# Kernel tuning notes

Hardware: AMD Instinct MI355X
Metric: run time of the kernel (lower is better)

The kernel has to match this reference:

```python
import jax, jax.numpy as jnp
import numpy as np

B, N, C, DIN, DOUT = 16, 65536, 256, 16, 16  # ratio = N // C = 256 nodes per cluster


def setup_inputs() -> dict:
    key = jax.random.key(0)
    k1, k2, k3, k4, k5 = jax.random.split(key, 5)
    stdv = 1.0 / np.sqrt(DOUT)
    x = jax.random.normal(k1, (B, N, DIN), dtype=jnp.float32)
    # parameters, pre-reshaped: torch w_diag (in*out, C) with out-major io axis -> (out, in, C)
    w_diag = jax.random.uniform(k2, (DOUT, DIN, C), jnp.float32, -stdv, stdv)
    w_off = jax.random.uniform(k3, (DOUT, DIN, C, C), jnp.float32, -stdv, stdv)
    b1 = jax.random.uniform(k4, (DOUT,), jnp.float32, -stdv, stdv)
    # flatten_ids(cluster_ids): a permutation putting each cluster's nodes contiguous
    permute_ids = jax.random.permutation(k5, N)
    return {"x": x, "w_diag": w_diag, "w_off": w_off, "b1": b1, "permute_ids": permute_ids}


def reference(x, w_diag, w_off, b1, permute_ids):
    # Faithful to: W = rearrange(kron(diag_embed(w_diag), I_r)) + (1/N) rearrange(kron(w_off, 1_{rxr}))
    # out = inv_permute( reshape( W @ flatten(permute(x)) ) ) + b1,
    # computed via the block-constant structure instead of materializing the (Dout*N, Din*N) W.
    Bq, Nn, Din = x.shape
    Dout, _, Cc = w_diag.shape
    ratio = Nn // Cc
    inv_permute = jnp.argsort(permute_ids)
    xp = x[:, permute_ids, :]                       # (B, N, Din), cluster-contiguous
    xc = xp.reshape(Bq, Cc, ratio, Din)             # (B, C, r, Din)
    # diagonal blocks: per-cluster Din->Dout mixing, identity over within-cluster index
    out_diag = jnp.einsum('oic,bcri->bcro', w_diag, xc)   # (B, C, r, Dout)
    # off blocks: constant within each (cluster j, cluster k) block -> use cluster sums
    s = xc.sum(axis=2)                              # (B, C, Din)
    out_off = jnp.einsum('oick,bki->bco', w_off, s) / Nn  # (B, C, Dout)
    out = out_diag + out_off[:, :, None, :]         # broadcast over within-cluster index
    out = out.reshape(Bq, Nn, Dout)[:, inv_permute, :] + b1[None, None, :]
    return out
```

## Files before the change

### kernel.cpp

```cpp
#include <hip/hip_runtime.h>

#define B_    16
#define N_    65536
#define C_    256
#define DIN_  16
#define DOUT_ 16

typedef float f32x4 __attribute__((ext_vector_type(4)));


__global__ __launch_bounds__(256) void k_sum_prep(
    const float* __restrict__ x, const float* __restrict__ w_diag,
    const int* __restrict__ P, const float* __restrict__ b1,
    float* __restrict__ s, float* __restrict__ wd_t,
    int* __restrict__ c_of_n, float* __restrict__ off)
{
    int bid = blockIdx.x;
    int t = threadIdx.x;
    if (bid >= B_ * C_) {
        int r = bid - B_ * C_;
        if (r < 256) {
            int o = r >> 4, i = r & 15;
            wd_t[t * 256 + i * 16 + o] = w_diag[r * C_ + t];
        } else if (r < 512) {
            int k = r - 256;
            c_of_n[P[k * 256 + t]] = k;
        } else {
            int m = (r - 512) * 256 + t;
            off[m] = b1[m & 15];
        }
        return;
    }
    int b = bid >> 8;
    int k = bid & (C_ - 1);
    int q  = t & 3;
    int rg = t >> 2;
    float4 acc = make_float4(0.f, 0.f, 0.f, 0.f);
    const int jbase = k << 8;
    #pragma unroll
    for (int m = 0; m < 4; ++m) {
        int n = P[jbase + rg + 64 * m];
        const float4* row =
            reinterpret_cast<const float4*>(x + ((size_t)(b * N_ + n)) * DIN_);
        float4 v = row[q];
        acc.x += v.x; acc.y += v.y; acc.z += v.z; acc.w += v.w;
    }
    #pragma unroll
    for (int mask = 4; mask <= 32; mask <<= 1) {
        acc.x += __shfl_xor(acc.x, mask, 64);
        acc.y += __shfl_xor(acc.y, mask, 64);
        acc.z += __shfl_xor(acc.z, mask, 64);
        acc.w += __shfl_xor(acc.w, mask, 64);
    }
    __shared__ float4 part[4][4];
    int lane = t & 63, wave = t >> 6;
    if (lane < 4) part[wave][lane] = acc;
    __syncthreads();
    if (t < 16) {
        int qq = t >> 2, comp = t & 3;
        float v = 0.f;
        #pragma unroll
        for (int w = 0; w < 4; ++w) {
            const float* p = reinterpret_cast<const float*>(&part[w][qq]);
            v += p[comp];
        }
        int i = qq * 4 + comp;
        s[(b * DIN_ + i) * C_ + k] = v;
    }
}

__global__ __launch_bounds__(256) void k_off(
    const float* __restrict__ w_off, const float* __restrict__ s,
    float* __restrict__ off)
{
    const int g  = (int)blockIdx.x;
    const int c  = g & 255;
    const int o0 = ((g >> 8) & 3) * 4;
    const int i0 = (g >> 10) * 4;
    const int t  = threadIdx.x;
    const int kq = t & 63;
    const int b0 = (t >> 6) * 4;

    const float4* w4 = reinterpret_cast<const float4*>(w_off);
    const float4* s4 = reinterpret_cast<const float4*>(s);

    float4 wv[4][4];
    float4 sv[4][4];
    #pragma unroll
    for (int ii = 0; ii < 4; ++ii) {
        const int i = i0 + ii;
        #pragma unroll
        for (int oo = 0; oo < 4; ++oo)
            wv[ii][oo] = w4[(((o0 + oo) * 16 + i) * 256 + c) * 64 + kq];
        #pragma unroll
        for (int bb = 0; bb < 4; ++bb)
            sv[ii][bb] = s4[((b0 + bb) * 16 + i) * 64 + kq];
    }
    __builtin_amdgcn_sched_barrier(0);

    float acc[16];
    #pragma unroll
    for (int z = 0; z < 16; ++z) acc[z] = 0.f;

    #pragma unroll
    for (int ii = 0; ii < 4; ++ii) {
        #pragma unroll
        for (int oo = 0; oo < 4; ++oo) {
            #pragma unroll
            for (int bb = 0; bb < 4; ++bb) {
                acc[oo * 4 + bb] += wv[ii][oo].x * sv[ii][bb].x
                                  + wv[ii][oo].y * sv[ii][bb].y
                                  + wv[ii][oo].z * sv[ii][bb].z
                                  + wv[ii][oo].w * sv[ii][bb].w;
            }
        }
    }

#define FOLD(MASK, CNT)                                                        \
    {                                                                          \
        const bool hi_ = (kq & (MASK)) != 0;                                   \
        _Pragma("unroll")                                                      \
        for (int j = 0; j < (CNT); ++j) {                                      \
            float keep = hi_ ? acc[j + (CNT)] : acc[j];                        \
            float send = hi_ ? acc[j] : acc[j + (CNT)];                        \
            acc[j] = keep + __shfl_xor(send, (MASK), 64);                      \
        }                                                                      \
    }
    FOLD(1, 8) FOLD(2, 4) FOLD(4, 2) FOLD(8, 1)
#undef FOLD
    acc[0] += __shfl_xor(acc[0], 16, 64);
    acc[0] += __shfl_xor(acc[0], 32, 64);

    if (kq < 16) {
        int j  = ((kq & 1) << 3) | ((kq & 2) << 1) | ((kq & 4) >> 1) | ((kq & 8) >> 3);
        int oo = j >> 2;
        int bb = j & 3;
        int b  = b0 + bb;
        int o  = o0 + oo;
        atomicAdd(&off[((b << 8) + c) * DOUT_ + o], acc[0] * (1.0f / (float)N_));
    }
}

__global__ __launch_bounds__(256) void k_apply_seq(
    const float* __restrict__ x, const int* __restrict__ c_of_n,
    const float* __restrict__ wd_t, const float* __restrict__ off,
    float* __restrict__ out)
{
    int t = threadIdx.x;
    int lr = t >> 2, q = t & 3;
    int n = blockIdx.x * 64 + lr;
    int c = c_of_n[n];

    const float4* wd4 = reinterpret_cast<const float4*>(wd_t);
    float4 wds[16];
    #pragma unroll
    for (int i = 0; i < 16; ++i) wds[i] = wd4[c * 64 + i * 4 + q];

    const float4* x4   = reinterpret_cast<const float4*>(x);
    const float4* off4 = reinterpret_cast<const float4*>(off);
    f32x4* out4        = reinterpret_cast<f32x4*>(out);

    #pragma unroll 2
    for (int b = 0; b < B_; ++b) {
        size_t rowbase = ((size_t)(b * N_ + n)) * 4;
        float4 x0 = x4[rowbase + 0];
        float4 x1 = x4[rowbase + 1];
        float4 x2 = x4[rowbase + 2];
        float4 x3 = x4[rowbase + 3];
        float4 acc = off4[((size_t)((b << 8) + c)) * 4 + q];
        float xv[16];
        xv[0]=x0.x; xv[1]=x0.y; xv[2]=x0.z; xv[3]=x0.w;
        xv[4]=x1.x; xv[5]=x1.y; xv[6]=x1.z; xv[7]=x1.w;
        xv[8]=x2.x; xv[9]=x2.y; xv[10]=x2.z; xv[11]=x2.w;
        xv[12]=x3.x; xv[13]=x3.y; xv[14]=x3.z; xv[15]=x3.w;
        #pragma unroll
        for (int i = 0; i < 16; ++i) {
            acc.x += xv[i] * wds[i].x;
            acc.y += xv[i] * wds[i].y;
            acc.z += xv[i] * wds[i].z;
            acc.w += xv[i] * wds[i].w;
        }
        f32x4 accv;
        accv.x = acc.x; accv.y = acc.y; accv.z = acc.z; accv.w = acc.w;
        __builtin_nontemporal_store(accv, &out4[rowbase + q]);
    }
}

extern "C" void kernel_launch(void* const* d_in, const int* in_sizes, int n_in,
                              void* d_out, int out_size, void* d_ws, size_t ws_size,
                              hipStream_t stream) {
    const float* x      = (const float*)d_in[0];
    const float* w_diag = (const float*)d_in[1];
    const float* w_off  = (const float*)d_in[2];
    const float* b1     = (const float*)d_in[3];
    const int*   P      = (const int*)d_in[4];
    float* out    = (float*)d_out;
    float* s      = (float*)d_ws;
    float* off    = s + 65536;
    float* wd_t   = off + 65536;
    int*   c_of_n = (int*)(wd_t + 65536);

    k_sum_prep<<<B_ * C_ + 768, 256, 0, stream>>>(x, w_diag, P, b1,
                                                  s, wd_t, c_of_n, off);
    k_off<<<4096, 256, 0, stream>>>(w_off, s, off);
    k_apply_seq<<<N_ / 64, 256, 0, stream>>>(x, c_of_n, wd_t, off, out);
}
```

Baseline: 197.3 us.

## Double-buffer w_off/s loads in k_off and double the input channels per block

k_off now has each block cover 8 input channels instead of 4, so it launches half as many blocks. The loop over input channels is software-pipelined with two register buffers: the loads for the next channel are issued before the FMAs for the current one, with sched barriers enforcing that order. The goal is to hide global-load latency on the large w_off stream and to halve the atomicAdd count on the off buffer. The cost is more registers per thread and fewer blocks available to fill the GPU.

```diff
diff --git a/kernel.cpp b/kernel.cpp
--- a/kernel.cpp
+++ b/kernel.cpp
@@ -75,8 +75,9 @@
 {
     const int g  = (int)blockIdx.x;
     const int c  = g & 255;
-    const int o0 = ((g >> 8) & 3) * 4;
-    const int i0 = (g >> 10) * 4;
+    const int r  = g >> 8;
+    const int o0 = (r & 3) * 4;
+    const int i0 = (r >> 2) * 8;
     const int t  = threadIdx.x;
     const int kq = t & 63;
     const int b0 = (t >> 6) * 4;
@@ -84,37 +85,52 @@
     const float4* w4 = reinterpret_cast<const float4*>(w_off);
     const float4* s4 = reinterpret_cast<const float4*>(s);
 
-    float4 wv[4][4];
-    float4 sv[4][4];
-    #pragma unroll
-    for (int ii = 0; ii < 4; ++ii) {
-        const int i = i0 + ii;
-        #pragma unroll
-        for (int oo = 0; oo < 4; ++oo)
-            wv[ii][oo] = w4[(((o0 + oo) * 16 + i) * 256 + c) * 64 + kq];
-        #pragma unroll
-        for (int bb = 0; bb < 4; ++bb)
-            sv[ii][bb] = s4[((b0 + bb) * 16 + i) * 64 + kq];
-    }
-    __builtin_amdgcn_sched_barrier(0);
+    const int wb = ((o0 * 16 + i0) * 256 + c) * 64 + kq;
+    const int sb = (b0 * 16 + i0) * 64 + kq;
 
     float acc[16];
     #pragma unroll
     for (int z = 0; z < 16; ++z) acc[z] = 0.f;
 
-    #pragma unroll
-    for (int ii = 0; ii < 4; ++ii) {
-        #pragma unroll
-        for (int oo = 0; oo < 4; ++oo) {
-            #pragma unroll
-            for (int bb = 0; bb < 4; ++bb) {
-                acc[oo * 4 + bb] += wv[ii][oo].x * sv[ii][bb].x
-                                  + wv[ii][oo].y * sv[ii][bb].y
-                                  + wv[ii][oo].z * sv[ii][bb].z
-                                  + wv[ii][oo].w * sv[ii][bb].w;
-            }
-        }
-    }
+    float4 wA0, wA1, wA2, wA3, sA0, sA1, sA2, sA3;
+    float4 wB0, wB1, wB2, wB3, sB0, sB1, sB2, sB3;
+
+#define LOADG(W0, W1, W2, W3, S0, S1, S2, S3, II)                              \
+    W0 = w4[wb + 0 * 262144 + (II) * 16384];                                   \
+    W1 = w4[wb + 1 * 262144 + (II) * 16384];                                   \
+    W2 = w4[wb + 2 * 262144 + (II) * 16384];                                   \
+    W3 = w4[wb + 3 * 262144 + (II) * 16384];                                   \
+    S0 = s4[sb + 0 * 1024 + (II) * 64];                                        \
+    S1 = s4[sb + 1 * 1024 + (II) * 64];                                        \
+    S2 = s4[sb + 2 * 1024 + (II) * 64];                                        \
+    S3 = s4[sb + 3 * 1024 + (II) * 64];
+
+#define FMAG(W0, W1, W2, W3, S0, S1, S2, S3)                                   \
+    {                                                                          \
+        const float4 ww[4] = {W0, W1, W2, W3};                                 \
+        const float4 ss[4] = {S0, S1, S2, S3};                                 \
+        _Pragma("unroll")                                                      \
+        for (int oo = 0; oo < 4; ++oo)                                         \
+            _Pragma("unroll")                                                  \
+            for (int bb = 0; bb < 4; ++bb)                                     \
+                acc[oo * 4 + bb] += ww[oo].x * ss[bb].x + ww[oo].y * ss[bb].y  \
+                                  + ww[oo].z * ss[bb].z + ww[oo].w * ss[bb].w; \
+    }
+
+    LOADG(wA0, wA1, wA2, wA3, sA0, sA1, sA2, sA3, 0)
+    #pragma unroll
+    for (int ii = 0; ii < 8; ii += 2) {
+        LOADG(wB0, wB1, wB2, wB3, sB0, sB1, sB2, sB3, ii + 1)
+        __builtin_amdgcn_sched_barrier(0);
+        FMAG(wA0, wA1, wA2, wA3, sA0, sA1, sA2, sA3)
+        if (ii + 2 < 8) {
+            LOADG(wA0, wA1, wA2, wA3, sA0, sA1, sA2, sA3, ii + 2)
+        }
+        __builtin_amdgcn_sched_barrier(0);
+        FMAG(wB0, wB1, wB2, wB3, sB0, sB1, sB2, sB3)
+    }
+#undef LOADG
+#undef FMAG
 
 #define FOLD(MASK, CNT)                                                        \
     {                                                                          \
@@ -202,6 +218,6 @@
 
     k_sum_prep<<<B_ * C_ + 768, 256, 0, stream>>>(x, w_diag, P, b1,
                                                   s, wd_t, c_of_n, off);
-    k_off<<<4096, 256, 0, stream>>>(w_off, s, off);
+    k_off<<<2048, 256, 0, stream>>>(w_off, s, off);
     k_apply_seq<<<N_ / 64, 256, 0, stream>>>(x, c_of_n, wd_t, off, out);
 }
```

Result: slower. 202.0 us (+2.4%).
